# Optimization experiments

Measured on AMD Instinct MI355X. Metric: run time of the kernel, lower is better.

The kernel has to match this reference:

```python
import jax, jax.numpy as jnp
import numpy as np

N = 3072          # in_features == out_features (CIFAR-10 flat dim)
BATCH = 8192
K_TOP = 16        # K selected pseudo-diagonals
ALPHA_LR = 0.01   # l in the Dykstra soft top-k
NUM_ITER = 50


def sparse_soft_topk_mask_dykstra(alpha, k, l, num_iter=NUM_ITER):
    """Differentiable sparse top-k mask (Sander et al. 2023, p=2):
    Euclidean projection of alpha/l onto the capped simplex
    {m : 0 <= m <= 1, sum(m) = k}, via Dykstra's alternating projections
    (hyperplane sum=k  <->  box [0,1]^n). Returns exact zeros off the top-k.
    """
    z = alpha / l
    n = z.shape[0]

    def body(carry, _):
        x, p, q = carry
        # project x + p onto hyperplane {sum = k}
        y = x + p
        y = y + (k - jnp.sum(y)) / n
        p = x + p - y
        # project y + q onto box [0, 1]^n
        xn = jnp.clip(y + q, 0.0, 1.0)
        q = y + q - xn
        return (xn, p, q), None

    init = (z, jnp.zeros_like(z), jnp.zeros_like(z))
    (x, _, _), _ = jax.lax.scan(body, init, None, length=num_iter)
    return x


def setup_inputs() -> dict:
    key = jax.random.key(0)
    k1, k2, k3 = jax.random.split(key, 3)
    x = jax.random.normal(k1, (BATCH, N), dtype=jnp.float32)
    # kaiming_uniform_(a=sqrt(5)) on (N, N): bound = sqrt(6/((1+5)*N)) = 1/sqrt(N)
    limit = 1.0 / float(np.sqrt(N))
    V = jax.random.uniform(k2, (N, N), jnp.float32, -limit, limit)
    alpha = jax.random.uniform(k3, (N,), jnp.float32)  # alpha >= 0 as asserted
    return {"x": x, "V": V, "alpha": alpha}


def reference(x, V, alpha):
    n = V.shape[0]
    a_topk = sparse_soft_topk_mask_dykstra(alpha, K_TOP, ALPHA_LR)
    # Pseudo-diagonal mask for diag i: ones at (row=(i+c) % n, col=c).
    # matmul(mask_i, diag(V[i])) scales column c by V[i, c], so
    #   W[r, c] = sum_i a_topk[i] * V[i, c] * [r == (i + c) % n]
    # i.e. exactly one i contributes per (r, c): i = (r - c) mod n.
    # a_topk is exactly zero off the top-k, so this gather equals the
    # original loop over nonzero indices without materializing masks.
    r = jnp.arange(n)
    idx = (r[:, None] - r[None, :]) % n          # (in, out) -> source diag i
    W = a_topk[idx] * V[idx, r[None, :]]          # (in, out)
    # F.linear(x, W): x @ W.T, x: (B, out) -> out: (B, in)
    return x @ W.T
```

## Files before the change

kernel.cpp:

```cpp
#include <hip/hip_runtime.h>
#include <hip/hip_bf16.h>
#include <stdint.h>

#define NDIM 3072
#define BATCHN 8192
#define KTOP 16.0f
#define NITER 50

typedef __attribute__((ext_vector_type(8))) short short8;
typedef __attribute__((ext_vector_type(4))) float floatx4;
typedef __attribute__((ext_vector_type(4))) unsigned short ushortx4;

__device__ inline unsigned short f2bf(float f) {
    __hip_bfloat16 h = __float2bfloat16(f);
    return *reinterpret_cast<unsigned short*>(&h);
}

__global__ void dykstra_kernel(const float* __restrict__ alpha, float* __restrict__ a_out) {
    const int lane = threadIdx.x;
    float z[48];
    float sl = 0.f;
#pragma unroll
    for (int e = 0; e < 48; ++e) {
        z[e] = alpha[e * 64 + lane] / 0.01f;
        sl += z[e];
    }
    float S = sl;
#pragma unroll
    for (int m = 1; m < 64; m <<= 1) S += __shfl_xor(S, m, 64);

    float D = 0.f;
    for (int it = 0; it < NITER; ++it) {
        D += (KTOP - S) / (float)NDIM;
        float s2 = 0.f;
#pragma unroll
        for (int e = 0; e < 48; ++e) {
            float v = z[e] + D;
            v = v < 0.f ? 0.f : (v > 1.f ? 1.f : v);
            s2 += v;
        }
        S = s2;
#pragma unroll
        for (int m = 1; m < 64; m <<= 1) S += __shfl_xor(S, m, 64);
    }
#pragma unroll
    for (int e = 0; e < 48; ++e) {
        float v = z[e] + D;
        v = v < 0.f ? 0.f : (v > 1.f ? 1.f : v);
        a_out[e * 64 + lane] = v;
    }
}

__global__ __launch_bounds__(256) void build_w(const float* __restrict__ V,
                                               const float* __restrict__ a,
                                               unsigned short* __restrict__ W) {
    __shared__ float Vs[128][64];
    __shared__ float as_[128];
    const int tid = threadIdx.x;
    const int c0 = blockIdx.x * 64;
    const int r0 = blockIdx.y * 64;
    int ib = r0 - c0 - 63;
    ib %= NDIM; if (ib < 0) ib += NDIM;

    if (tid < 128) {
        int i = ib + tid; if (i >= NDIM) i -= NDIM;
        as_[tid] = a[i];
    }
#pragma unroll
    for (int it = 0; it < 32; ++it) {
        int idx = it * 256 + tid;
        int d = idx >> 6, cc = idx & 63;
        int i = ib + d; if (i >= NDIM) i -= NDIM;
        Vs[d][cc] = V[(size_t)i * NDIM + c0 + cc];
    }
    __syncthreads();

    const int cc = tid & 63;
    const int rrb = (tid >> 6) * 16;
#pragma unroll
    for (int p = 0; p < 16; ++p) {
        int rr = rrb + p;
        int d = rr - cc + 63;
        float v = as_[d] * Vs[d][cc];
        W[(size_t)(r0 + rr) * NDIM + (c0 + cc)] = f2bf(v);
    }
}

__global__ void convert_x(const float* __restrict__ x, unsigned short* __restrict__ xb, int n) {
    int i = (blockIdx.x * blockDim.x + threadIdx.x) * 4;
    const int stride = gridDim.x * blockDim.x * 4;
    for (; i < n; i += stride) {
        floatx4 v = *(const floatx4*)(x + i);
        ushortx4 o;
        o[0] = f2bf(v[0]); o[1] = f2bf(v[1]); o[2] = f2bf(v[2]); o[3] = f2bf(v[3]);
        *(ushortx4*)(xb + i) = o;
    }
}

#define BM 128
#define BN 128
#define BK 64

__global__ __launch_bounds__(256) void gemm_bt(const unsigned short* __restrict__ A,
                                               const unsigned short* __restrict__ B,
                                               float* __restrict__ C,
                                               int M, int N, int K, int ntiles_n) {
    __shared__ __align__(16) unsigned short As[BM * BK];
    __shared__ __align__(16) unsigned short Bs[BN * BK];

    const int nwg = gridDim.x;
    const int cpx = nwg >> 3;
    const int bid = blockIdx.x;
    const int swz = (bid & 7) * cpx + (bid >> 3);
    const int tm = swz / ntiles_n, tn = swz % ntiles_n;
    const int m0 = tm * BM, n0 = tn * BN;

    const int tid = threadIdx.x;
    const int lane = tid & 63;
    const int wid = tid >> 6;
    const int wm = wid >> 1, wn = wid & 1;

    floatx4 acc[4][4];
#pragma unroll
    for (int i = 0; i < 4; ++i)
#pragma unroll
        for (int j = 0; j < 4; ++j) acc[i][j] = {0.f, 0.f, 0.f, 0.f};

    const unsigned short* Ab = A + (size_t)m0 * K;
    const unsigned short* Bb = B + (size_t)n0 * K;

    for (int kt = 0; kt < K; kt += BK) {
        __syncthreads();
#pragma unroll
        for (int li = 0; li < 4; ++li) {
            int off = li * 4096 + tid * 16;
            int row = off >> 7;
            int col = (off & 127) >> 1;
            const unsigned short* g = Ab + (size_t)row * K + kt + col;
            __builtin_amdgcn_global_load_lds(
                (const __attribute__((address_space(1))) unsigned int*)g,
                (__attribute__((address_space(3))) unsigned int*)((char*)As + off),
                16, 0, 0);
        }
#pragma unroll
        for (int li = 0; li < 4; ++li) {
            int off = li * 4096 + tid * 16;
            int row = off >> 7;
            int col = (off & 127) >> 1;
            const unsigned short* g = Bb + (size_t)row * K + kt + col;
            __builtin_amdgcn_global_load_lds(
                (const __attribute__((address_space(1))) unsigned int*)g,
                (__attribute__((address_space(3))) unsigned int*)((char*)Bs + off),
                16, 0, 0);
        }
        asm volatile("s_waitcnt vmcnt(0)" ::: "memory");
        __syncthreads();

#pragma unroll
        for (int ks = 0; ks < 2; ++ks) {
            short8 af[4], bf[4];
#pragma unroll
            for (int mi = 0; mi < 4; ++mi) {
                int r = wm * 64 + mi * 16 + (lane & 15);
                int c = ks * 32 + (lane >> 4) * 8;
                af[mi] = *(const short8*)&As[r * BK + c];
            }
#pragma unroll
            for (int ni = 0; ni < 4; ++ni) {
                int r = wn * 64 + ni * 16 + (lane & 15);
                int c = ks * 32 + (lane >> 4) * 8;
                bf[ni] = *(const short8*)&Bs[r * BK + c];
            }
#pragma unroll
            for (int mi = 0; mi < 4; ++mi)
#pragma unroll
                for (int ni = 0; ni < 4; ++ni)
                    acc[mi][ni] = __builtin_amdgcn_mfma_f32_16x16x32_bf16(af[mi], bf[ni], acc[mi][ni], 0, 0, 0);
        }
    }

#pragma unroll
    for (int mi = 0; mi < 4; ++mi)
#pragma unroll
        for (int ni = 0; ni < 4; ++ni)
#pragma unroll
            for (int rg = 0; rg < 4; ++rg) {
                int rr = m0 + wm * 64 + mi * 16 + (lane >> 4) * 4 + rg;
                int cc = n0 + wn * 64 + ni * 16 + (lane & 15);
                C[(size_t)rr * N + cc] = acc[mi][ni][rg];
            }
}

extern "C" void kernel_launch(void* const* d_in, const int* in_sizes, int n_in,
                              void* d_out, int out_size, void* d_ws, size_t ws_size,
                              hipStream_t stream) {
    const float* x     = (const float*)d_in[0];
    const float* V     = (const float*)d_in[1];
    const float* alpha = (const float*)d_in[2];
    float* out = (float*)d_out;

    float* a_ws = (float*)d_ws;
    unsigned short* xb = (unsigned short*)((char*)d_ws + 16384);
    unsigned short* Wb = (unsigned short*)((char*)d_ws + 16384 + (size_t)BATCHN * NDIM * 2);

    hipLaunchKernelGGL(dykstra_kernel, dim3(1), dim3(64), 0, stream, alpha, a_ws);
    hipLaunchKernelGGL(build_w, dim3(NDIM / 64, NDIM / 64), dim3(256), 0, stream, V, a_ws, Wb);
    hipLaunchKernelGGL(convert_x, dim3(2048), dim3(256), 0, stream, x, xb, BATCHN * NDIM);
    hipLaunchKernelGGL(gemm_bt, dim3((BATCHN / BM) * (NDIM / BN)), dim3(256), 0, stream,
                       xb, Wb, out, BATCHN, NDIM, NDIM, NDIM / BN);
}
```

Measured before the change: 462.8 us.

## Pipeline GEMM with 4-slot LDS ring, BK=32, and vectorize build_w

The GEMM now uses a four-slot LDS ring buffer with BK=32 and issues global-to-LDS loads three tiles ahead, gated by counted vmcnt waits instead of full drains. The shared-memory layout is rearranged so each wave's MFMA fragments are contiguous 16-byte reads, and s_setprio is raised around the MFMA block. The tile swizzle is hardcoded to M-major order. build_w is vectorized to float4 loads and 4-wide bf16 stores. The aim is to hide global load latency behind MFMA work, at the cost of extra barriers per iteration and more LDS per block (64KB).

```diff
diff --git a/kernel.cpp b/kernel.cpp
--- a/kernel.cpp
+++ b/kernel.cpp
@@ -7,6 +7,13 @@
 #define KTOP 16.0f
 #define NITER 50
 
+#define BM 128
+#define BN 128
+#define BK 32
+#define NT (NDIM / BK)
+#define SLOT_BYTES 16384
+#define ABYTES 8192
+
 typedef __attribute__((ext_vector_type(8))) short short8;
 typedef __attribute__((ext_vector_type(4))) float floatx4;
 typedef __attribute__((ext_vector_type(4))) unsigned short ushortx4;
@@ -19,13 +26,11 @@
 __global__ void dykstra_kernel(const float* __restrict__ alpha, float* __restrict__ a_out) {
     const int lane = threadIdx.x;
     float z[48];
-    float sl = 0.f;
-#pragma unroll
-    for (int e = 0; e < 48; ++e) {
-        z[e] = alpha[e * 64 + lane] / 0.01f;
-        sl += z[e];
-    }
-    float S = sl;
+#pragma unroll
+    for (int e = 0; e < 48; ++e) z[e] = alpha[e * 64 + lane] / 0.01f;
+    float S = 0.f;
+#pragma unroll
+    for (int e = 0; e < 48; ++e) S += z[e];
 #pragma unroll
     for (int m = 1; m < 64; m <<= 1) S += __shfl_xor(S, m, 64);
 
@@ -67,22 +72,28 @@
         as_[tid] = a[i];
     }
 #pragma unroll
-    for (int it = 0; it < 32; ++it) {
+    for (int it = 0; it < 8; ++it) {
         int idx = it * 256 + tid;
-        int d = idx >> 6, cc = idx & 63;
+        int d = idx >> 4;
+        int c4 = (idx & 15) * 4;
         int i = ib + d; if (i >= NDIM) i -= NDIM;
-        Vs[d][cc] = V[(size_t)i * NDIM + c0 + cc];
+        *(floatx4*)&Vs[d][c4] = *(const floatx4*)&V[(size_t)i * NDIM + c0 + c4];
     }
     __syncthreads();
 
-    const int cc = tid & 63;
-    const int rrb = (tid >> 6) * 16;
-#pragma unroll
-    for (int p = 0; p < 16; ++p) {
-        int rr = rrb + p;
-        int d = rr - cc + 63;
-        float v = as_[d] * Vs[d][cc];
-        W[(size_t)(r0 + rr) * NDIM + (c0 + cc)] = f2bf(v);
+    const int c4 = (tid & 15) * 4;
+    const int rr0 = tid >> 4;
+#pragma unroll
+    for (int p = 0; p < 4; ++p) {
+        int rr = p * 16 + rr0;
+        ushortx4 o;
+#pragma unroll
+        for (int j = 0; j < 4; ++j) {
+            int cc = c4 + j;
+            int d = rr - cc + 63;
+            o[j] = f2bf(as_[d] * Vs[d][cc]);
+        }
+        *(ushortx4*)&W[(size_t)(r0 + rr) * NDIM + (c0 + c4)] = o;
     }
 }
 
@@ -97,22 +108,15 @@
     }
 }
 
-#define BM 128
-#define BN 128
-#define BK 64
-
-__global__ __launch_bounds__(256) void gemm_bt(const unsigned short* __restrict__ A,
-                                               const unsigned short* __restrict__ B,
-                                               float* __restrict__ C,
-                                               int M, int N, int K, int ntiles_n) {
-    __shared__ __align__(16) unsigned short As[BM * BK];
-    __shared__ __align__(16) unsigned short Bs[BN * BK];
-
-    const int nwg = gridDim.x;
-    const int cpx = nwg >> 3;
+__global__ __launch_bounds__(256, 2) void gemm_bt(const unsigned short* __restrict__ A,
+                                                  const unsigned short* __restrict__ B,
+                                                  float* __restrict__ C) {
+    __shared__ __align__(16) char lds[4 * SLOT_BYTES];
+
     const int bid = blockIdx.x;
-    const int swz = (bid & 7) * cpx + (bid >> 3);
-    const int tm = swz / ntiles_n, tn = swz % ntiles_n;
+    const int swz = (bid & 7) * 192 + (bid >> 3);
+    const int tm = swz & 63;
+    const int tn = swz >> 6;
     const int m0 = tm * BM, n0 = tn * BN;
 
     const int tid = threadIdx.x;
@@ -120,63 +124,69 @@
     const int wid = tid >> 6;
     const int wm = wid >> 1, wn = wid & 1;
 
+    const unsigned short* Ab = A + (size_t)m0 * NDIM;
+    const unsigned short* Bb = B + (size_t)n0 * NDIM;
+
+    const int sblk = tid >> 6;
+    const int srow = lane & 15;
+    const int scol = (lane >> 4) * 8;
+
     floatx4 acc[4][4];
 #pragma unroll
     for (int i = 0; i < 4; ++i)
 #pragma unroll
         for (int j = 0; j < 4; ++j) acc[i][j] = {0.f, 0.f, 0.f, 0.f};
 
-    const unsigned short* Ab = A + (size_t)m0 * K;
-    const unsigned short* Bb = B + (size_t)n0 * K;
-
-    for (int kt = 0; kt < K; kt += BK) {
-        __syncthreads();
-#pragma unroll
-        for (int li = 0; li < 4; ++li) {
-            int off = li * 4096 + tid * 16;
-            int row = off >> 7;
-            int col = (off & 127) >> 1;
-            const unsigned short* g = Ab + (size_t)row * K + kt + col;
+    auto STAGE = [&](int T) {
+        char* sb = lds + (T & 3) * SLOT_BYTES;
+        const int kt = T * BK;
+#pragma unroll
+        for (int r = 0; r < 2; ++r) {
+            const unsigned short* g = Ab + (size_t)((r * 4 + sblk) * 16 + srow) * NDIM + kt + scol;
             __builtin_amdgcn_global_load_lds(
                 (const __attribute__((address_space(1))) unsigned int*)g,
-                (__attribute__((address_space(3))) unsigned int*)((char*)As + off),
+                (__attribute__((address_space(3))) unsigned int*)(sb + r * 4096 + tid * 16),
                 16, 0, 0);
         }
 #pragma unroll
-        for (int li = 0; li < 4; ++li) {
-            int off = li * 4096 + tid * 16;
-            int row = off >> 7;
-            int col = (off & 127) >> 1;
-            const unsigned short* g = Bb + (size_t)row * K + kt + col;
+        for (int r = 0; r < 2; ++r) {
+            const unsigned short* g = Bb + (size_t)((r * 4 + sblk) * 16 + srow) * NDIM + kt + scol;
             __builtin_amdgcn_global_load_lds(
                 (const __attribute__((address_space(1))) unsigned int*)g,
-                (__attribute__((address_space(3))) unsigned int*)((char*)Bs + off),
+                (__attribute__((address_space(3))) unsigned int*)(sb + ABYTES + r * 4096 + tid * 16),
                 16, 0, 0);
         }
-        asm volatile("s_waitcnt vmcnt(0)" ::: "memory");
-        __syncthreads();
-
-#pragma unroll
-        for (int ks = 0; ks < 2; ++ks) {
-            short8 af[4], bf[4];
-#pragma unroll
-            for (int mi = 0; mi < 4; ++mi) {
-                int r = wm * 64 + mi * 16 + (lane & 15);
-                int c = ks * 32 + (lane >> 4) * 8;
-                af[mi] = *(const short8*)&As[r * BK + c];
-            }
-#pragma unroll
-            for (int ni = 0; ni < 4; ++ni) {
-                int r = wn * 64 + ni * 16 + (lane & 15);
-                int c = ks * 32 + (lane >> 4) * 8;
-                bf[ni] = *(const short8*)&Bs[r * BK + c];
-            }
-#pragma unroll
-            for (int mi = 0; mi < 4; ++mi)
-#pragma unroll
-                for (int ni = 0; ni < 4; ++ni)
-                    acc[mi][ni] = __builtin_amdgcn_mfma_f32_16x16x32_bf16(af[mi], bf[ni], acc[mi][ni], 0, 0, 0);
-        }
+    };
+
+    STAGE(0); STAGE(1); STAGE(2);
+    asm volatile("s_waitcnt vmcnt(8)" ::: "memory");
+    asm volatile("s_barrier" ::: "memory");
+
+    for (int T = 0; T < NT; ++T) {
+        const char* sb = lds + (T & 3) * SLOT_BYTES;
+        short8 af[4], bf[4];
+#pragma unroll
+        for (int mi = 0; mi < 4; ++mi)
+            af[mi] = *(const short8*)(sb + (wm * 4 + mi) * 1024 + lane * 16);
+#pragma unroll
+        for (int ni = 0; ni < 4; ++ni)
+            bf[ni] = *(const short8*)(sb + ABYTES + (wn * 4 + ni) * 1024 + lane * 16);
+
+        if (T + 3 < NT) STAGE(T + 3);
+
+        if (T < NT - 3)       { asm volatile("s_waitcnt vmcnt(8)" ::: "memory"); }
+        else if (T == NT - 3) { asm volatile("s_waitcnt vmcnt(4)" ::: "memory"); }
+        else if (T == NT - 2) { asm volatile("s_waitcnt vmcnt(0)" ::: "memory"); }
+        asm volatile("s_barrier" ::: "memory");
+
+        __builtin_amdgcn_s_setprio(1);
+#pragma unroll
+        for (int mi = 0; mi < 4; ++mi)
+#pragma unroll
+            for (int ni = 0; ni < 4; ++ni)
+                acc[mi][ni] = __builtin_amdgcn_mfma_f32_16x16x32_bf16(af[mi], bf[ni], acc[mi][ni], 0, 0, 0);
+        __builtin_amdgcn_s_setprio(0);
+        asm volatile("s_barrier" ::: "memory");
     }
 
 #pragma unroll
@@ -187,7 +197,7 @@
             for (int rg = 0; rg < 4; ++rg) {
                 int rr = m0 + wm * 64 + mi * 16 + (lane >> 4) * 4 + rg;
                 int cc = n0 + wn * 64 + ni * 16 + (lane & 15);
-                C[(size_t)rr * N + cc] = acc[mi][ni][rg];
+                C[(size_t)rr * NDIM + cc] = acc[mi][ni][rg];
             }
 }
 
@@ -207,5 +217,5 @@
     hipLaunchKernelGGL(build_w, dim3(NDIM / 64, NDIM / 64), dim3(256), 0, stream, V, a_ws, Wb);
     hipLaunchKernelGGL(convert_x, dim3(2048), dim3(256), 0, stream, x, xb, BATCHN * NDIM);
     hipLaunchKernelGGL(gemm_bt, dim3((BATCHN / BM) * (NDIM / BN)), dim3(256), 0, stream,
-                       xb, Wb, out, BATCHN, NDIM, NDIM, NDIM / BN);
-}
+                       xb, Wb, out);
+}
```

Result: slower. 523.2 us (+13.0%).
